# Performance work log

Hardware: AMD Instinct MI355X
Metric: run time of the kernel (lower is better)

The kernel has to match this reference:

```python
import jax, jax.numpy as jnp
import numpy as np

E, N = 400000, 50000
D = 128          # efeat_dim = src_dim = dst_dim = output_dim
H = 512          # hidden_dim
CAT = 3 * D      # concat of [efeat, src, dst]
LN_EPS = 1e-5


def setup_inputs() -> dict:
    key = jax.random.key(0)
    ks = jax.random.split(key, 12)
    scale = 0.02
    return {
        "efeat": jax.random.normal(ks[0], (E, D), jnp.float32),
        "src_feat": jax.random.normal(ks[1], (N, D), jnp.float32),
        "dst_feat": jax.random.normal(ks[2], (N, D), jnp.float32),
        "src_idx": jax.random.randint(ks[3], (E,), 0, N),
        "dst_idx": jax.random.randint(ks[4], (E,), 0, N),
        # MLP params: Linear(CAT,H) -> SiLU -> Linear(H,H) -> SiLU -> Linear(H,D) -> LayerNorm(D)
        "W1": jax.random.normal(ks[5], (CAT, H), jnp.float32) * scale,
        "b1": jnp.zeros((H,), jnp.float32),
        "W2": jax.random.normal(ks[6], (H, H), jnp.float32) * scale,
        "b2": jnp.zeros((H,), jnp.float32),
        "W3": jax.random.normal(ks[7], (H, D), jnp.float32) * scale,
        "b3": jnp.zeros((D,), jnp.float32),
        "gamma": jnp.ones((D,), jnp.float32),
        "beta": jnp.zeros((D,), jnp.float32),
    }


def _layer_norm(y, gamma, beta):
    mu = jnp.mean(y, axis=-1, keepdims=True)
    var = jnp.mean(jnp.square(y - mu), axis=-1, keepdims=True)
    return (y - mu) * jax.lax.rsqrt(var + LN_EPS) * gamma + beta


def reference(efeat, src_feat, dst_feat, src_idx, dst_idx,
              W1, b1, W2, b2, W3, b3, gamma, beta):
    # concat_efeat: per-edge gather of src/dst node feats + concat with edge feats
    cat = jnp.concatenate([efeat, src_feat[src_idx], dst_feat[dst_idx]], axis=1)  # [E, 3D]
    h = jax.nn.silu(cat @ W1 + b1)   # [E, H]
    h = jax.nn.silu(h @ W2 + b2)     # [E, H]
    y = h @ W3 + b3                  # [E, D]
    return _layer_norm(y, gamma, beta)
```

## Files before the change

### kernel.cpp

```cpp
#include <hip/hip_runtime.h>
#include <hip/hip_bf16.h>
#include <cstdint>
#include <cstddef>

typedef __attribute__((ext_vector_type(4))) float f32x4;
typedef __attribute__((ext_vector_type(8))) short s16x8;

#define E_ 400000
#define D_ 128
#define H_ 512
#define CAT_ 384
#define BM 96
#define NBLK 4167

#define CATPITCH 40
#define CATSLOT (BM * CATPITCH * 2)
#define CATBASE 98304
#define LDS_TOTAL (CATBASE + 5 * CATSLOT)

__device__ __forceinline__ unsigned short f2bf(float x) {
  union { float f; unsigned u; } t; t.f = x;
  return (unsigned short)((t.u + 0x8000u) >> 16);
}
__device__ __forceinline__ float silu_f(float x) {
  return x * __builtin_amdgcn_rcpf(1.0f + __expf(-x));
}

#define HS(row, byteoff) (smem + (row) * 1024 + ((byteoff) ^ (((row) & 7) << 4)))

__global__ __launch_bounds__(512, 2)
void edge_mlp_fused(const float* __restrict__ efeat,
                    const float* __restrict__ src_feat,
                    const float* __restrict__ dst_feat,
                    const int* __restrict__ src_idx,
                    const int* __restrict__ dst_idx,
                    const unsigned short* __restrict__ P1,
                    const unsigned short* __restrict__ P2,
                    const unsigned short* __restrict__ P3,
                    const float* __restrict__ b1,
                    const float* __restrict__ b2,
                    const float* __restrict__ b3,
                    const float* __restrict__ gamma,
                    const float* __restrict__ beta,
                    float* __restrict__ out) {
  extern __shared__ char smem[];
  const int tid = threadIdx.x;
  const int lane = tid & 63;
  const int wave = tid >> 6;
  const int lr = lane & 15;
  const int kc = lane >> 4;
  const int g4 = kc * 4;
  const size_t e0 = (size_t)blockIdx.x * BM;
  const int rem = (int)((size_t)E_ - e0 < (size_t)BM ? (size_t)E_ - e0 : (size_t)BM);

  const int grow = tid >> 2, gq = tid & 3;
  const float* gb0 = nullptr; const float* gb1 = nullptr; const float* gb2 = nullptr;
  if (tid < 384) {
    const int gr = grow < rem ? grow : rem - 1;
    const size_t ee = e0 + gr;
    gb0 = efeat + ee * D_;
    gb1 = src_feat + (size_t)src_idx[ee] * D_;
    gb2 = dst_feat + (size_t)dst_idx[ee] * D_;
  }
  f32x4 ga[2][2];

#define CGLOAD(P, S) { const float* s_ = ((P) < 4 ? gb0 : (P) < 8 ? gb1 : gb2) + ((P) & 3) * 32 + gq * 8; \
                       ga[S][0] = *(const f32x4*)s_; ga[S][1] = *(const f32x4*)(s_ + 4); }
#define CPWRITE(P, S) { unsigned short* d_ = (unsigned short*)(smem + CATBASE + ((P) % 5) * CATSLOT) + grow * CATPITCH + gq * 8; \
                        ushort4 w_; \
                        w_.x = f2bf(ga[S][0][0]); w_.y = f2bf(ga[S][0][1]); \
                        w_.z = f2bf(ga[S][0][2]); w_.w = f2bf(ga[S][0][3]); \
                        *(ushort4*)d_ = w_; \
                        w_.x = f2bf(ga[S][1][0]); w_.y = f2bf(ga[S][1][1]); \
                        w_.z = f2bf(ga[S][1][2]); w_.w = f2bf(ga[S][1][3]); \
                        *(ushort4*)(d_ + 4) = w_; }

  const unsigned short* w1base = P1 + (size_t)kc * 4096 + wave * 512 + lr * 8;
  const unsigned short* w2base = P2 + (size_t)kc * 4096 + wave * 512 + lr * 8;
  const unsigned short* w3base = P3 + (size_t)kc * 1024 + lr * 8;

  {
    f32x4 acc[6][4];
    #pragma unroll
    for (int eg = 0; eg < 6; ++eg)
      #pragma unroll
      for (int j = 0; j < 4; ++j) acc[eg][j] = (f32x4){0.f, 0.f, 0.f, 0.f};

    s16x8 w1r[2][4];
    if (tid < 384) {
      CGLOAD(0, 0); CPWRITE(0, 0);
      CGLOAD(1, 1); CPWRITE(1, 1);
      CGLOAD(2, 0); CPWRITE(2, 0);
      CGLOAD(3, 1);
    }
    #pragma unroll
    for (int j = 0; j < 4; ++j) w1r[0][j] = *(const s16x8*)(w1base + j * 128);

    asm volatile("s_waitcnt lgkmcnt(0)" ::: "memory");
    __builtin_amdgcn_s_barrier();
    asm volatile("" ::: "memory");

    #pragma unroll
    for (int p = 0; p < 12; ++p) {
      if (tid < 384) {
        if (p <= 8) CPWRITE(p + 3, (p + 1) & 1);
        if (p <= 7) CGLOAD(p + 4, p & 1);
      }
      if (p <= 10) {
        #pragma unroll
        for (int j = 0; j < 4; ++j)
          w1r[(p + 1) & 1][j] = *(const s16x8*)(w1base + (size_t)(p + 1) * 16384 + j * 128);
      }
      asm volatile("s_waitcnt lgkmcnt(0)" ::: "memory");
      __builtin_amdgcn_s_barrier();
      asm volatile("" ::: "memory");

      const unsigned short* cp = (const unsigned short*)(smem + CATBASE + (p % 5) * CATSLOT);
      s16x8 bf[6];
      #pragma unroll
      for (int eg = 0; eg < 6; ++eg)
        bf[eg] = *(const s16x8*)(cp + (eg * 16 + lr) * CATPITCH + kc * 8);
      #pragma unroll
      for (int j = 0; j < 4; ++j)
        #pragma unroll
        for (int eg = 0; eg < 6; ++eg)
          acc[eg][j] = __builtin_amdgcn_mfma_f32_16x16x32_bf16(w1r[p & 1][j], bf[eg], acc[eg][j], 0, 0, 0);
    }

    #pragma unroll
    for (int j = 0; j < 4; ++j) {
      const int col0 = (wave * 4 + j) * 16 + g4;
      const f32x4 bv = *(const f32x4*)(b1 + col0);
      #pragma unroll
      for (int eg = 0; eg < 6; ++eg) {
        ushort4 w_;
        w_.x = f2bf(silu_f(acc[eg][j][0] + bv[0]));
        w_.y = f2bf(silu_f(acc[eg][j][1] + bv[1]));
        w_.z = f2bf(silu_f(acc[eg][j][2] + bv[2]));
        w_.w = f2bf(silu_f(acc[eg][j][3] + bv[3]));
        *(ushort4*)HS(eg * 16 + lr, col0 * 2) = w_;
      }
    }
  }
  __syncthreads();

  {
    f32x4 acc[6][4];
    #pragma unroll
    for (int eg = 0; eg < 6; ++eg)
      #pragma unroll
      for (int j = 0; j < 4; ++j) acc[eg][j] = (f32x4){0.f, 0.f, 0.f, 0.f};

    s16x8 w2r[2][4];
    #pragma unroll
    for (int j = 0; j < 4; ++j) w2r[0][j] = *(const s16x8*)(w2base + j * 128);

    #pragma unroll
    for (int p = 0; p < 16; ++p) {
      if (p <= 14) {
        #pragma unroll
        for (int j = 0; j < 4; ++j)
          w2r[(p + 1) & 1][j] = *(const s16x8*)(w2base + (size_t)(p + 1) * 16384 + j * 128);
      }
      s16x8 bf[6];
      #pragma unroll
      for (int eg = 0; eg < 6; ++eg)
        bf[eg] = *(const s16x8*)HS(eg * 16 + lr, p * 64 + kc * 16);
      #pragma unroll
      for (int j = 0; j < 4; ++j)
        #pragma unroll
        for (int eg = 0; eg < 6; ++eg)
          acc[eg][j] = __builtin_amdgcn_mfma_f32_16x16x32_bf16(w2r[p & 1][j], bf[eg], acc[eg][j], 0, 0, 0);
    }
    __syncthreads();

    #pragma unroll
    for (int j = 0; j < 4; ++j) {
      const int col0 = (wave * 4 + j) * 16 + g4;
      const f32x4 bv = *(const f32x4*)(b2 + col0);
      #pragma unroll
      for (int eg = 0; eg < 6; ++eg) {
        ushort4 w_;
        w_.x = f2bf(silu_f(acc[eg][j][0] + bv[0]));
        w_.y = f2bf(silu_f(acc[eg][j][1] + bv[1]));
        w_.z = f2bf(silu_f(acc[eg][j][2] + bv[2]));
        w_.w = f2bf(silu_f(acc[eg][j][3] + bv[3]));
        *(ushort4*)HS(eg * 16 + lr, col0 * 2) = w_;
      }
    }
  }
  __syncthreads();

  if (wave < 6) {
    f32x4 acc[8];
    #pragma unroll
    for (int f = 0; f < 8; ++f) acc[f] = (f32x4){0.f, 0.f, 0.f, 0.f};

    s16x8 w3r[2][8];
    #pragma unroll
    for (int f = 0; f < 8; ++f) w3r[0][f] = *(const s16x8*)(w3base + f * 128);

    #pragma unroll
    for (int p = 0; p < 16; ++p) {
      if (p <= 14) {
        #pragma unroll
        for (int f = 0; f < 8; ++f)
          w3r[(p + 1) & 1][f] = *(const s16x8*)(w3base + (size_t)(p + 1) * 4096 + f * 128);
      }
      const s16x8 bf = *(const s16x8*)HS(wave * 16 + lr, p * 64 + kc * 16);
      #pragma unroll
      for (int f = 0; f < 8; ++f)
        acc[f] = __builtin_amdgcn_mfma_f32_16x16x32_bf16(w3r[p & 1][f], bf, acc[f], 0, 0, 0);
    }

    const int edge = wave * 16 + lr;
    float sum = 0.f, ss = 0.f;
    #pragma unroll
    for (int f = 0; f < 8; ++f) {
      const f32x4 bv = *(const f32x4*)(b3 + f * 16 + g4);
      #pragma unroll
      for (int r = 0; r < 4; ++r) {
        acc[f][r] += bv[r];
        sum += acc[f][r];
        ss += acc[f][r] * acc[f][r];
      }
    }
    sum += __shfl_xor(sum, 16, 64); ss += __shfl_xor(ss, 16, 64);
    sum += __shfl_xor(sum, 32, 64); ss += __shfl_xor(ss, 32, 64);
    const float mu = sum * (1.0f / 128.0f);
    const float var = ss * (1.0f / 128.0f) - mu * mu;
    const float rstd = rsqrtf(var + 1e-5f);
    if (edge < rem) {
      float* orow = out + (e0 + edge) * D_;
      #pragma unroll
      for (int f = 0; f < 8; ++f) {
        const f32x4 gv = *(const f32x4*)(gamma + f * 16 + g4);
        const f32x4 btv = *(const f32x4*)(beta + f * 16 + g4);
        f32x4 o;
        #pragma unroll
        for (int r = 0; r < 4; ++r)
          o[r] = (acc[f][r] - mu) * rstd * gv[r] + btv[r];
        *(f32x4*)(orow + f * 16 + g4) = o;
      }
    }
  }
#undef CGLOAD
#undef CPWRITE
}

__global__ void prep_pack(const float* __restrict__ W, unsigned short* __restrict__ P,
                          int K, int N) {
  const int t = blockIdx.x * blockDim.x + threadIdx.x;
  if (t >= N * (K >> 3)) return;
  const int n = t % N;
  const int k8 = t / N;
  const int k0 = k8 << 3;
  const int p = k0 >> 5, kc = (k0 >> 3) & 3;
  s16x8 w;
  #pragma unroll
  for (int j = 0; j < 8; ++j)
    w[j] = (short)f2bf(W[(size_t)(k0 + j) * N + n]);
  *(s16x8*)(P + (size_t)p * N * 32 + (size_t)kc * N * 8 + (size_t)n * 8) = w;
}

extern "C" void kernel_launch(void* const* d_in, const int* in_sizes, int n_in,
                              void* d_out, int out_size, void* d_ws, size_t ws_size,
                              hipStream_t stream) {
  const float* efeat    = (const float*)d_in[0];
  const float* src_feat = (const float*)d_in[1];
  const float* dst_feat = (const float*)d_in[2];
  const int*   src_idx  = (const int*)d_in[3];
  const int*   dst_idx  = (const int*)d_in[4];
  const float* W1 = (const float*)d_in[5];
  const float* b1 = (const float*)d_in[6];
  const float* W2 = (const float*)d_in[7];
  const float* b2 = (const float*)d_in[8];
  const float* W3 = (const float*)d_in[9];
  const float* b3 = (const float*)d_in[10];
  const float* gamma = (const float*)d_in[11];
  const float* beta  = (const float*)d_in[12];

  unsigned short* P1 = (unsigned short*)d_ws;
  unsigned short* P2 = P1 + 196608;
  unsigned short* P3 = P2 + 262144;

  (void)hipFuncSetAttribute((const void*)edge_mlp_fused,
                            hipFuncAttributeMaxDynamicSharedMemorySize, LDS_TOTAL);

  prep_pack<<<(512 * 48 + 255) / 256, 256, 0, stream>>>(W1, P1, CAT_, H_);
  prep_pack<<<(512 * 64 + 255) / 256, 256, 0, stream>>>(W2, P2, H_, H_);
  prep_pack<<<(128 * 64 + 255) / 256, 256, 0, stream>>>(W3, P3, H_, D_);

  edge_mlp_fused<<<NBLK, 512, LDS_TOTAL, stream>>>(
      efeat, src_feat, dst_feat, src_idx, dst_idx,
      P1, P2, P3, b1, b2, b3, gamma, beta, (float*)d_out);
}
```

Before: 603.2 us.

## Shrink edge tile to 64 and pack four blocks per CU

Reduces the edge tile from 96 to 64 rows so LDS per block fits in 64 KB, with the cat ring buffer moved to overlap the tail of the hidden buffer, and raises launch bounds to four blocks per CU. Weight register double-buffering is dropped in favour of loading weights at each k-step, and all 512 threads now share the gather work. Tail guards are removed since 64 divides E exactly. The aim is more waves resident per CU to hide gather and weight-load latency. In exchange each block reuses every weight fetch across fewer edges, and register pressure is tighter under the higher occupancy bound.

```diff
diff --git a/kernel.cpp b/kernel.cpp
--- a/kernel.cpp
+++ b/kernel.cpp
@@ -10,13 +10,13 @@
 #define D_ 128
 #define H_ 512
 #define CAT_ 384
-#define BM 96
-#define NBLK 4167
+#define BM 64
+#define NBLK 6250
 
 #define CATPITCH 40
 #define CATSLOT (BM * CATPITCH * 2)
-#define CATBASE 98304
-#define LDS_TOTAL (CATBASE + 5 * CATSLOT)
+#define RINGBASE (65536 - 5 * CATSLOT)
+#define LDS_TOTAL 65536
 
 __device__ __forceinline__ unsigned short f2bf(float x) {
   union { float f; unsigned u; } t; t.f = x;
@@ -28,7 +28,7 @@
 
 #define HS(row, byteoff) (smem + (row) * 1024 + ((byteoff) ^ (((row) & 7) << 4)))
 
-__global__ __launch_bounds__(512, 2)
+__global__ __launch_bounds__(512, 4)
 void edge_mlp_fused(const float* __restrict__ efeat,
                     const float* __restrict__ src_feat,
                     const float* __restrict__ dst_feat,
@@ -51,50 +51,37 @@
   const int kc = lane >> 4;
   const int g4 = kc * 4;
   const size_t e0 = (size_t)blockIdx.x * BM;
-  const int rem = (int)((size_t)E_ - e0 < (size_t)BM ? (size_t)E_ - e0 : (size_t)BM);
-
-  const int grow = tid >> 2, gq = tid & 3;
-  const float* gb0 = nullptr; const float* gb1 = nullptr; const float* gb2 = nullptr;
-  if (tid < 384) {
-    const int gr = grow < rem ? grow : rem - 1;
-    const size_t ee = e0 + gr;
-    gb0 = efeat + ee * D_;
-    gb1 = src_feat + (size_t)src_idx[ee] * D_;
-    gb2 = dst_feat + (size_t)dst_idx[ee] * D_;
-  }
-  f32x4 ga[2][2];
-
-#define CGLOAD(P, S) { const float* s_ = ((P) < 4 ? gb0 : (P) < 8 ? gb1 : gb2) + ((P) & 3) * 32 + gq * 8; \
-                       ga[S][0] = *(const f32x4*)s_; ga[S][1] = *(const f32x4*)(s_ + 4); }
-#define CPWRITE(P, S) { unsigned short* d_ = (unsigned short*)(smem + CATBASE + ((P) % 5) * CATSLOT) + grow * CATPITCH + gq * 8; \
-                        ushort4 w_; \
-                        w_.x = f2bf(ga[S][0][0]); w_.y = f2bf(ga[S][0][1]); \
-                        w_.z = f2bf(ga[S][0][2]); w_.w = f2bf(ga[S][0][3]); \
-                        *(ushort4*)d_ = w_; \
-                        w_.x = f2bf(ga[S][1][0]); w_.y = f2bf(ga[S][1][1]); \
-                        w_.z = f2bf(ga[S][1][2]); w_.w = f2bf(ga[S][1][3]); \
-                        *(ushort4*)(d_ + 4) = w_; }
+
+  const int grow = tid >> 3, gq = tid & 7;
+  const size_t ee = e0 + grow;
+  const float* gb0 = efeat + ee * D_;
+  const float* gb1 = src_feat + (size_t)src_idx[ee] * D_;
+  const float* gb2 = dst_feat + (size_t)dst_idx[ee] * D_;
+  f32x4 ga[2];
+
+#define CGLOAD(P) { ga[(P) & 1] = *(const f32x4*)(((P) < 4 ? gb0 : (P) < 8 ? gb1 : gb2) + ((P) & 3) * 32 + gq * 4); }
+#define CPWRITE(P) { unsigned short* d_ = (unsigned short*)(smem + RINGBASE + ((P) % 5) * CATSLOT) + grow * CATPITCH + gq * 4; \
+                     const f32x4 v_ = ga[(P) & 1]; \
+                     ushort4 w_; \
+                     w_.x = f2bf(v_[0]); w_.y = f2bf(v_[1]); \
+                     w_.z = f2bf(v_[2]); w_.w = f2bf(v_[3]); \
+                     *(ushort4*)d_ = w_; }
 
   const unsigned short* w1base = P1 + (size_t)kc * 4096 + wave * 512 + lr * 8;
   const unsigned short* w2base = P2 + (size_t)kc * 4096 + wave * 512 + lr * 8;
   const unsigned short* w3base = P3 + (size_t)kc * 1024 + lr * 8;
 
   {
-    f32x4 acc[6][4];
-    #pragma unroll
-    for (int eg = 0; eg < 6; ++eg)
+    f32x4 acc[4][4];
+    #pragma unroll
+    for (int eg = 0; eg < 4; ++eg)
       #pragma unroll
       for (int j = 0; j < 4; ++j) acc[eg][j] = (f32x4){0.f, 0.f, 0.f, 0.f};
 
-    s16x8 w1r[2][4];
-    if (tid < 384) {
-      CGLOAD(0, 0); CPWRITE(0, 0);
-      CGLOAD(1, 1); CPWRITE(1, 1);
-      CGLOAD(2, 0); CPWRITE(2, 0);
-      CGLOAD(3, 1);
-    }
-    #pragma unroll
-    for (int j = 0; j < 4; ++j) w1r[0][j] = *(const s16x8*)(w1base + j * 128);
+    CGLOAD(0); CPWRITE(0);
+    CGLOAD(1); CPWRITE(1);
+    CGLOAD(2); CPWRITE(2);
+    CGLOAD(3);
 
     asm volatile("s_waitcnt lgkmcnt(0)" ::: "memory");
     __builtin_amdgcn_s_barrier();
@@ -102,37 +89,36 @@
 
     #pragma unroll
     for (int p = 0; p < 12; ++p) {
-      if (tid < 384) {
-        if (p <= 8) CPWRITE(p + 3, (p + 1) & 1);
-        if (p <= 7) CGLOAD(p + 4, p & 1);
-      }
-      if (p <= 10) {
-        #pragma unroll
-        for (int j = 0; j < 4; ++j)
-          w1r[(p + 1) & 1][j] = *(const s16x8*)(w1base + (size_t)(p + 1) * 16384 + j * 128);
-      }
+      s16x8 w[4];
+      #pragma unroll
+      for (int j = 0; j < 4; ++j)
+        w[j] = *(const s16x8*)(w1base + (size_t)p * 16384 + j * 128);
+
+      if (p <= 8) { CPWRITE(p + 3); if (p <= 7) CGLOAD(p + 4); }
+
       asm volatile("s_waitcnt lgkmcnt(0)" ::: "memory");
       __builtin_amdgcn_s_barrier();
       asm volatile("" ::: "memory");
 
-      const unsigned short* cp = (const unsigned short*)(smem + CATBASE + (p % 5) * CATSLOT);
-      s16x8 bf[6];
-      #pragma unroll
-      for (int eg = 0; eg < 6; ++eg)
-        bf[eg] = *(const s16x8*)(cp + (eg * 16 + lr) * CATPITCH + kc * 8);
-      #pragma unroll
-      for (int j = 0; j < 4; ++j)
+      const unsigned short* cp = (const unsigned short*)(smem + RINGBASE + (p % 5) * CATSLOT);
+      #pragma unroll
+      for (int eg = 0; eg < 4; ++eg) {
+        const s16x8 bf = *(const s16x8*)(cp + (eg * 16 + lr) * CATPITCH + kc * 8);
         #pragma unroll
-        for (int eg = 0; eg < 6; ++eg)
-          acc[eg][j] = __builtin_amdgcn_mfma_f32_16x16x32_bf16(w1r[p & 1][j], bf[eg], acc[eg][j], 0, 0, 0);
-    }
+        for (int j = 0; j < 4; ++j)
+          acc[eg][j] = __builtin_amdgcn_mfma_f32_16x16x32_bf16(w[j], bf, acc[eg][j], 0, 0, 0);
+      }
+    }
+
+    __builtin_amdgcn_s_barrier();
+    asm volatile("" ::: "memory");
 
     #pragma unroll
     for (int j = 0; j < 4; ++j) {
       const int col0 = (wave * 4 + j) * 16 + g4;
       const f32x4 bv = *(const f32x4*)(b1 + col0);
       #pragma unroll
-      for (int eg = 0; eg < 6; ++eg) {
+      for (int eg = 0; eg < 4; ++eg) {
         ushort4 w_;
         w_.x = f2bf(silu_f(acc[eg][j][0] + bv[0]));
         w_.y = f2bf(silu_f(acc[eg][j][1] + bv[1]));
@@ -145,32 +131,25 @@
   __syncthreads();
 
   {
-    f32x4 acc[6][4];
-    #pragma unroll
-    for (int eg = 0; eg < 6; ++eg)
+    f32x4 acc[4][4];
+    #pragma unroll
+    for (int eg = 0; eg < 4; ++eg)
       #pragma unroll
       for (int j = 0; j < 4; ++j) acc[eg][j] = (f32x4){0.f, 0.f, 0.f, 0.f};
 
-    s16x8 w2r[2][4];
-    #pragma unroll
-    for (int j = 0; j < 4; ++j) w2r[0][j] = *(const s16x8*)(w2base + j * 128);
-
     #pragma unroll
     for (int p = 0; p < 16; ++p) {
-      if (p <= 14) {
+      s16x8 w[4];
+      #pragma unroll
+      for (int j = 0; j < 4; ++j)
+        w[j] = *(const s16x8*)(w2base + (size_t)p * 16384 + j * 128);
+      #pragma unroll
+      for (int eg = 0; eg < 4; ++eg) {
+        const s16x8 bf = *(const s16x8*)HS(eg * 16 + lr, p * 64 + kc * 16);
         #pragma unroll
         for (int j = 0; j < 4; ++j)
-          w2r[(p + 1) & 1][j] = *(const s16x8*)(w2base + (size_t)(p + 1) * 16384 + j * 128);
-      }
-      s16x8 bf[6];
-      #pragma unroll
-      for (int eg = 0; eg < 6; ++eg)
-        bf[eg] = *(const s16x8*)HS(eg * 16 + lr, p * 64 + kc * 16);
-      #pragma unroll
-      for (int j = 0; j < 4; ++j)
-        #pragma unroll
-        for (int eg = 0; eg < 6; ++eg)
-          acc[eg][j] = __builtin_amdgcn_mfma_f32_16x16x32_bf16(w2r[p & 1][j], bf[eg], acc[eg][j], 0, 0, 0);
+          acc[eg][j] = __builtin_amdgcn_mfma_f32_16x16x32_bf16(w[j], bf, acc[eg][j], 0, 0, 0);
+      }
     }
     __syncthreads();
 
@@ -179,7 +158,7 @@
       const int col0 = (wave * 4 + j) * 16 + g4;
       const f32x4 bv = *(const f32x4*)(b2 + col0);
       #pragma unroll
-      for (int eg = 0; eg < 6; ++eg) {
+      for (int eg = 0; eg < 4; ++eg) {
         ushort4 w_;
         w_.x = f2bf(silu_f(acc[eg][j][0] + bv[0]));
         w_.y = f2bf(silu_f(acc[eg][j][1] + bv[1]));
@@ -191,26 +170,21 @@
   }
   __syncthreads();
 
-  if (wave < 6) {
+  if (wave < 4) {
     f32x4 acc[8];
     #pragma unroll
     for (int f = 0; f < 8; ++f) acc[f] = (f32x4){0.f, 0.f, 0.f, 0.f};
 
-    s16x8 w3r[2][8];
-    #pragma unroll
-    for (int f = 0; f < 8; ++f) w3r[0][f] = *(const s16x8*)(w3base + f * 128);
-
     #pragma unroll
     for (int p = 0; p < 16; ++p) {
-      if (p <= 14) {
-        #pragma unroll
-        for (int f = 0; f < 8; ++f)
-          w3r[(p + 1) & 1][f] = *(const s16x8*)(w3base + (size_t)(p + 1) * 4096 + f * 128);
-      }
+      s16x8 w[8];
+      #pragma unroll
+      for (int f = 0; f < 8; ++f)
+        w[f] = *(const s16x8*)(w3base + (size_t)p * 4096 + f * 128);
       const s16x8 bf = *(const s16x8*)HS(wave * 16 + lr, p * 64 + kc * 16);
       #pragma unroll
       for (int f = 0; f < 8; ++f)
-        acc[f] = __builtin_amdgcn_mfma_f32_16x16x32_bf16(w3r[p & 1][f], bf, acc[f], 0, 0, 0);
+        acc[f] = __builtin_amdgcn_mfma_f32_16x16x32_bf16(w[f], bf, acc[f], 0, 0, 0);
     }
 
     const int edge = wave * 16 + lr;
@@ -230,18 +204,16 @@
     const float mu = sum * (1.0f / 128.0f);
     const float var = ss * (1.0f / 128.0f) - mu * mu;
     const float rstd = rsqrtf(var + 1e-5f);
-    if (edge < rem) {
-      float* orow = out + (e0 + edge) * D_;
-      #pragma unroll
-      for (int f = 0; f < 8; ++f) {
-        const f32x4 gv = *(const f32x4*)(gamma + f * 16 + g4);
-        const f32x4 btv = *(const f32x4*)(beta + f * 16 + g4);
-        f32x4 o;
-        #pragma unroll
-        for (int r = 0; r < 4; ++r)
-          o[r] = (acc[f][r] - mu) * rstd * gv[r] + btv[r];
-        *(f32x4*)(orow + f * 16 + g4) = o;
-      }
+    float* orow = out + (e0 + edge) * D_;
+    #pragma unroll
+    for (int f = 0; f < 8; ++f) {
+      const f32x4 gv = *(const f32x4*)(gamma + f * 16 + g4);
+      const f32x4 btv = *(const f32x4*)(beta + f * 16 + g4);
+      f32x4 o;
+      #pragma unroll
+      for (int r = 0; r < 4; ++r)
+        o[r] = (acc[f][r] - mu) * rstd * gv[r] + btv[r];
+      *(f32x4*)(orow + f * 16 + g4) = o;
     }
   }
 #undef CGLOAD
```

After: 572.0 us. 5.2% less time.
